# Kernel tuning notes

Hardware: AMD Instinct MI355X
Metric: run time of the kernel (lower is better)

The kernel has to match this reference:

```python
import jax, jax.numpy as jnp
import numpy as np

ALPHA = 4.0   # spikingjelly surrogate.Sigmoid default
TAU = 2.0
VTH = 1.0
EPS = 1e-5

@jax.custom_vjp
def spike(x):
    return (x >= 0.0).astype(x.dtype)

def _spike_fwd(x):
    return spike(x), x

def _spike_bwd(x, g):
    s = jax.nn.sigmoid(ALPHA * x)
    return (g * ALPHA * s * (1.0 - s),)

spike.defvjp(_spike_fwd, _spike_bwd)

def lif(x):
    # x: [T, B, N, C]; multi-step LIF, v_reset=0 hard reset, detach_reset=True
    def step(v, xt):
        v = v + (xt - v) / TAU          # charge
        s = spike(v - VTH)              # fire (surrogate grad)
        v = v * (1.0 - jax.lax.stop_gradient(s))  # hard reset, detached
        return v, s
    _, out = jax.lax.scan(step, jnp.zeros_like(x[0]), x)
    return out

def bn(x, gamma, beta):
    # BatchNorm1d in training mode: per-channel (last dim) over all other dims
    mu = x.mean(axis=(0, 1, 2), keepdims=True)
    var = x.var(axis=(0, 1, 2), keepdims=True)  # biased var, as torch BN uses for normalization
    return (x - mu) * jax.lax.rsqrt(var + EPS) * gamma + beta

def setup_inputs() -> dict:
    key = jax.random.key(0)
    ks = jax.random.split(key, 3)
    T, B, N, C, H = 4, 32, 1024, 256, 256
    x = jax.random.normal(ks[0], (T, B, N, C), dtype=jnp.float32)
    W1 = jax.random.normal(ks[1], (C, H), dtype=jnp.float32) * (1.0 / np.sqrt(C))
    W2 = jax.random.normal(ks[2], (H, C), dtype=jnp.float32) * (1.0 / np.sqrt(H))
    return {
        "x": x,
        "W1": W1, "b1": jnp.zeros((H,), jnp.float32),
        "gamma1": jnp.ones((H,), jnp.float32), "beta1": jnp.zeros((H,), jnp.float32),
        "W2": W2, "b2": jnp.zeros((C,), jnp.float32),
        "gamma2": jnp.ones((C,), jnp.float32), "beta2": jnp.zeros((C,), jnp.float32),
    }

def reference(x, W1, b1, gamma1, beta1, W2, b2, gamma2, beta2):
    # fc1: Linear -> BN (per-channel over T*B*N) -> multi-step LIF
    h = jnp.einsum('tbnc,ch->tbnh', x, W1) + b1
    h = lif(bn(h, gamma1, beta1))
    # fc2
    o = jnp.einsum('tbnh,ho->tbno', h, W2) + b2
    return lif(bn(o, gamma2, beta2))
```

## Files before the change

kernel.cpp:

```cpp
#include <hip/hip_runtime.h>


typedef __attribute__((ext_vector_type(8))) short bf16x8;
typedef __attribute__((ext_vector_type(8))) _Float16 f16x8;
typedef __attribute__((ext_vector_type(4))) _Float16 f16x4;
typedef __attribute__((ext_vector_type(4))) float f32x4;

__device__ __forceinline__ unsigned short f32_to_bf16_rne(float f) {
    unsigned int u = __builtin_bit_cast(unsigned int, f);
    u += 0x7FFFu + ((u >> 16) & 1u);
    return (unsigned short)(u >> 16);
}
__device__ __forceinline__ float bf16_to_f32(unsigned short h) {
    unsigned int u = ((unsigned int)h) << 16;
    return __builtin_bit_cast(float, u);
}

__global__ __launch_bounds__(256) void split_w1(const float* __restrict__ W1,
                                                _Float16* __restrict__ BhiT,
                                                _Float16* __restrict__ BloT) {
    int i = blockIdx.x * 256 + threadIdx.x;
    int k = i >> 8, n = i & 255;
    float w = W1[i];
    _Float16 hi = (_Float16)w;
    _Float16 lo = (_Float16)((w - (float)hi) * 4096.0f);
    BhiT[(size_t)n * 256 + k] = hi;
    BloT[(size_t)n * 256 + k] = lo;
}

__global__ __launch_bounds__(256) void split_w2(const float* __restrict__ W2,
                                                unsigned short* __restrict__ Bt) {
    int i = blockIdx.x * 256 + threadIdx.x;
    int k = i >> 8, n = i & 255;
    float w = W2[i];
    unsigned short hi = f32_to_bf16_rne(w);
    float r = w - bf16_to_f32(hi);
    unsigned short mid = f32_to_bf16_rne(r);
    float r2 = r - bf16_to_f32(mid);
    unsigned short lo = f32_to_bf16_rne(r2);
    Bt[(size_t)(0 * 256 + n) * 256 + k] = hi;
    Bt[(size_t)(1 * 256 + n) * 256 + k] = mid;
    Bt[(size_t)(2 * 256 + n) * 256 + k] = lo;
}

__global__ __launch_bounds__(512) void gemm1_mfma(const float* __restrict__ A,
                                                  const _Float16* __restrict__ Bhi,
                                                  const _Float16* __restrict__ Blo,
                                                  const float* __restrict__ bias,
                                                  float* __restrict__ C,
                                                  double* __restrict__ partial) {
    __shared__ __align__(16) _Float16 Ahi[128 * 256];
    __shared__ __align__(16) _Float16 Alo[128 * 256];
    const size_t m0 = (size_t)blockIdx.x * 128;
    const int tid = threadIdx.x;
    const int lane = tid & 63;
    const int wave = tid >> 6;
    const int wr = wave >> 2;
    const int wc = wave & 3;
    const int lrow = lane & 15, lchunk = lane >> 4;

    const _Float16* BhiB = Bhi + ((size_t)(64 * wc + lrow)) * 256 + lchunk * 8;
    const _Float16* BloB = Blo + ((size_t)(64 * wc + lrow)) * 256 + lchunk * 8;

    f16x8 bh[2][4], bl[2][4];
#define LOADB1(buf, kk)                                                   \
    _Pragma("unroll") for (int nf = 0; nf < 4; ++nf) {                    \
        bh[buf][nf] = *(const f16x8*)(BhiB + nf * 4096 + (kk) * 32);      \
        bl[buf][nf] = *(const f16x8*)(BloB + nf * 4096 + (kk) * 32);      \
    }

    LOADB1(0, 0)

    {
        const float* src = A + m0 * 256;
#pragma unroll
        for (int it = 0; it < 16; ++it) {
            unsigned i4 = (unsigned)(it * 512 + tid);
            float4 v = *(const float4*)(src + (size_t)i4 * 4);
            float f[4] = {v.x, v.y, v.z, v.w};
            f16x4 hi4, lo4;
#pragma unroll
            for (int e = 0; e < 4; ++e) {
                _Float16 hh = (_Float16)f[e];
                hi4[e] = hh;
                lo4[e] = (_Float16)((f[e] - (float)hh) * 4096.0f);
            }
            unsigned off = i4 * 8u;
            unsigned swz = off ^ (((off >> 9) & 7u) << 4);
            *(f16x4*)((char*)Ahi + swz) = hi4;
            *(f16x4*)((char*)Alo + swz) = lo4;
        }
    }
    __syncthreads();

    f32x4 acc0[4][4] = {}, acc1[4][4] = {};

#pragma unroll
    for (int k0 = 0; k0 < 8; ++k0) {
        const int cur = k0 & 1;
        if (k0 < 7) { LOADB1(cur ^ 1, k0 + 1) }
        f16x8 ah[4], al[4];
#pragma unroll
        for (int mf = 0; mf < 4; ++mf) {
            unsigned r = (unsigned)(64 * wr + 16 * mf + lrow);
            unsigned off = (r * 512u + (unsigned)(k0 * 64 + lchunk * 16)) ^ ((r & 7u) << 4);
            ah[mf] = *(const f16x8*)((const char*)Ahi + off);
            al[mf] = *(const f16x8*)((const char*)Alo + off);
        }
#pragma unroll
        for (int nf = 0; nf < 4; ++nf)
#pragma unroll
            for (int mf = 0; mf < 4; ++mf)
                acc0[mf][nf] = __builtin_amdgcn_mfma_f32_16x16x32_f16(
                    ah[mf], bh[cur][nf], acc0[mf][nf], 0, 0, 0);
#pragma unroll
        for (int nf = 0; nf < 4; ++nf)
#pragma unroll
            for (int mf = 0; mf < 4; ++mf)
                acc1[mf][nf] = __builtin_amdgcn_mfma_f32_16x16x32_f16(
                    ah[mf], bl[cur][nf], acc1[mf][nf], 0, 0, 0);
#pragma unroll
        for (int nf = 0; nf < 4; ++nf)
#pragma unroll
            for (int mf = 0; mf < 4; ++mf)
                acc1[mf][nf] = __builtin_amdgcn_mfma_f32_16x16x32_f16(
                    al[mf], bh[cur][nf], acc1[mf][nf], 0, 0, 0);
    }
#undef LOADB1

    const float UNSCALE = 1.0f / 4096.0f;
    double s[4], q[4];
#pragma unroll
    for (int nf = 0; nf < 4; ++nf) {
        int col = 64 * wc + 16 * nf + lrow;
        float bvv = bias[col];
        double ss = 0.0, qq = 0.0;
#pragma unroll
        for (int mf = 0; mf < 4; ++mf) {
            size_t rowb = m0 + 64 * wr + 16 * mf + 4 * lchunk;
#pragma unroll
            for (int e = 0; e < 4; ++e) {
                float hv = acc0[mf][nf][e] + acc1[mf][nf][e] * UNSCALE + bvv;
                C[(rowb + e) * 256 + col] = hv;
                ss += (double)hv;
                qq += (double)hv * (double)hv;
            }
        }
        s[nf] = ss;
        q[nf] = qq;
    }
#pragma unroll
    for (int nf = 0; nf < 4; ++nf) {
        s[nf] += __shfl_xor(s[nf], 16);
        s[nf] += __shfl_xor(s[nf], 32);
        q[nf] += __shfl_xor(q[nf], 16);
        q[nf] += __shfl_xor(q[nf], 32);
    }
    __syncthreads();
    double* shred = (double*)Ahi;
    if (lane < 16) {
#pragma unroll
        for (int nf = 0; nf < 4; ++nf) {
            shred[(wave * 4 + nf) * 16 + lane] = s[nf];
            shred[512 + (wave * 4 + nf) * 16 + lane] = q[nf];
        }
    }
    __syncthreads();
    if (wave < 4) {
        int nf = lane >> 4, lr = lane & 15;
        int col = 64 * wave + 16 * nf + lr;
        double ssum = shred[(wave * 4 + nf) * 16 + lr] +
                      shred[((4 + wave) * 4 + nf) * 16 + lr];
        double qsum = shred[512 + (wave * 4 + nf) * 16 + lr] +
                      shred[512 + ((4 + wave) * 4 + nf) * 16 + lr];
        partial[(size_t)col * 1024 + blockIdx.x] = ssum;
        partial[(size_t)(256 + col) * 1024 + blockIdx.x] = qsum;
    }
}

__global__ __launch_bounds__(512) void gemm2_mfma(const unsigned short* __restrict__ A,
                                                  const unsigned short* __restrict__ Bt,
                                                  const float* __restrict__ bias,
                                                  float* __restrict__ C,
                                                  double* __restrict__ partial) {
    __shared__ __align__(16) unsigned short Asw[128 * 256];
    const size_t m0 = (size_t)blockIdx.x * 128;
    const int tid = threadIdx.x;
    const int lane = tid & 63;
    const int wave = tid >> 6;
    const int wr = wave >> 2;
    const int wc = wave & 3;
    const int lrow = lane & 15, lchunk = lane >> 4;

    {
        const char* src = (const char*)(A + m0 * 256);
        char* dst = (char*)Asw;
#pragma unroll
        for (int it = 0; it < 8; ++it) {
            unsigned off = (unsigned)(it * 512 + tid) * 16u;
            float4 v = *(const float4*)(src + off);
            unsigned swz = off ^ (((off >> 9) & 7u) << 4);
            *(float4*)(dst + swz) = v;
        }
    }

    const unsigned short* Bbase =
        Bt + ((size_t)(64 * wc + lrow)) * 256 + lchunk * 8;

    bf16x8 bb[2][12];
#define LOADB(buf, kk)                                                        \
    _Pragma("unroll") for (int t = 0; t < 3; ++t)                             \
    _Pragma("unroll") for (int nf = 0; nf < 4; ++nf)                          \
        bb[buf][t * 4 + nf] = *(const bf16x8*)(Bbase + (size_t)t * 65536 +    \
                                               nf * 4096 + (kk) * 32);

    LOADB(0, 0)
    __syncthreads();

    f32x4 acc[4][4] = {};

#pragma unroll
    for (int k0 = 0; k0 < 8; ++k0) {
        const int cur = k0 & 1;
        if (k0 < 7) { LOADB(cur ^ 1, k0 + 1) }
        bf16x8 af[4];
#pragma unroll
        for (int mf = 0; mf < 4; ++mf) {
            unsigned r = (unsigned)(64 * wr + 16 * mf + lrow);
            unsigned off = r * 512u + (unsigned)(k0 * 64 + lchunk * 16);
            off ^= ((r & 7u) << 4);
            af[mf] = *(const bf16x8*)((const char*)Asw + off);
        }
#pragma unroll
        for (int t = 0; t < 3; ++t)
#pragma unroll
            for (int nf = 0; nf < 4; ++nf)
#pragma unroll
                for (int mf = 0; mf < 4; ++mf)
                    acc[mf][nf] = __builtin_amdgcn_mfma_f32_16x16x32_bf16(
                        af[mf], bb[cur][t * 4 + nf], acc[mf][nf], 0, 0, 0);
    }
#undef LOADB

    double s[4], q[4];
#pragma unroll
    for (int nf = 0; nf < 4; ++nf) {
        int col = 64 * wc + 16 * nf + lrow;
        float bvv = bias[col];
        double ss = 0.0, qq = 0.0;
#pragma unroll
        for (int mf = 0; mf < 4; ++mf) {
            size_t rowb = m0 + 64 * wr + 16 * mf + 4 * lchunk;
#pragma unroll
            for (int e = 0; e < 4; ++e) {
                float hv = acc[mf][nf][e] + bvv;
                C[(rowb + e) * 256 + col] = hv;
                ss += (double)hv;
                qq += (double)hv * (double)hv;
            }
        }
        s[nf] = ss;
        q[nf] = qq;
    }
#pragma unroll
    for (int nf = 0; nf < 4; ++nf) {
        s[nf] += __shfl_xor(s[nf], 16);
        s[nf] += __shfl_xor(s[nf], 32);
        q[nf] += __shfl_xor(q[nf], 16);
        q[nf] += __shfl_xor(q[nf], 32);
    }
    __syncthreads();
    double* shred = (double*)Asw;
    if (lane < 16) {
#pragma unroll
        for (int nf = 0; nf < 4; ++nf) {
            shred[(wave * 4 + nf) * 16 + lane] = s[nf];
            shred[512 + (wave * 4 + nf) * 16 + lane] = q[nf];
        }
    }
    __syncthreads();
    if (wave < 4) {
        int nf = lane >> 4, lr = lane & 15;
        int col = 64 * wave + 16 * nf + lr;
        double ssum = shred[(wave * 4 + nf) * 16 + lr] +
                      shred[((4 + wave) * 4 + nf) * 16 + lr];
        double qsum = shred[512 + (wave * 4 + nf) * 16 + lr] +
                      shred[512 + ((4 + wave) * 4 + nf) * 16 + lr];
        partial[(size_t)col * 1024 + blockIdx.x] = ssum;
        partial[(size_t)(256 + col) * 1024 + blockIdx.x] = qsum;
    }
}

__global__ __launch_bounds__(256) void finalize_stats(const double* __restrict__ partial,
                                                      const float* __restrict__ gamma,
                                                      const float* __restrict__ beta,
                                                      float2* __restrict__ ss,
                                                      int nblocks, double invM) {
    const int c = blockIdx.x;
    const int t = threadIdx.x;
    __shared__ double sh[256];
    __shared__ double sh2[256];
    double s = 0.0, s2 = 0.0;
    for (int b = t; b < nblocks; b += 256) {
        s += partial[(size_t)c * nblocks + b];
        s2 += partial[(size_t)(256 + c) * nblocks + b];
    }
    sh[t] = s;
    sh2[t] = s2;
    __syncthreads();
#pragma unroll
    for (int off = 128; off > 0; off >>= 1) {
        if (t < off) {
            sh[t] += sh[t + off];
            sh2[t] += sh2[t + off];
        }
        __syncthreads();
    }
    if (t == 0) {
        double mu = sh[0] * invM;
        double var = sh2[0] * invM - mu * mu;
        double rstd = 1.0 / sqrt(var + 1e-5);
        double sc = (double)gamma[c] * rstd;
        ss[c] = make_float2((float)sc, (float)((double)beta[c] - mu * sc));
    }
}

__global__ __launch_bounds__(256) void bnlif_bf16(const float* __restrict__ h,
                                                  const float2* __restrict__ ss,
                                                  unsigned short* __restrict__ out,
                                                  int slab4) {
    int t4 = blockIdx.x * 256 + threadIdx.x;
    if (t4 >= slab4) return;
    size_t idx = (size_t)t4 * 4;
    int c0 = (int)(idx & 255);
    float2 p0 = ss[c0], p1 = ss[c0 + 1], p2 = ss[c0 + 2], p3 = ss[c0 + 3];
    size_t slab = (size_t)slab4 * 4;
    float4 v = make_float4(0.f, 0.f, 0.f, 0.f);
#pragma unroll
    for (int t = 0; t < 4; ++t) {
        float4 hv = *(const float4*)(h + (size_t)t * slab + idx);
        float x0 = hv.x * p0.x + p0.y;
        float x1 = hv.y * p1.x + p1.y;
        float x2 = hv.z * p2.x + p2.y;
        float x3 = hv.w * p3.x + p3.y;
        v.x = v.x + (x0 - v.x) * 0.5f;
        v.y = v.y + (x1 - v.y) * 0.5f;
        v.z = v.z + (x2 - v.z) * 0.5f;
        v.w = v.w + (x3 - v.w) * 0.5f;
        ushort4 sp;
        sp.x = (v.x >= 1.0f) ? 0x3F80 : 0;
        sp.y = (v.y >= 1.0f) ? 0x3F80 : 0;
        sp.z = (v.z >= 1.0f) ? 0x3F80 : 0;
        sp.w = (v.w >= 1.0f) ? 0x3F80 : 0;
        v.x = (v.x >= 1.0f) ? 0.0f : v.x;
        v.y = (v.y >= 1.0f) ? 0.0f : v.y;
        v.z = (v.z >= 1.0f) ? 0.0f : v.z;
        v.w = (v.w >= 1.0f) ? 0.0f : v.w;
        *(ushort4*)(out + (size_t)t * slab + idx) = sp;
    }
}

__global__ __launch_bounds__(256) void bnlif_f32(const float* __restrict__ h,
                                                 const float2* __restrict__ ss,
                                                 float* __restrict__ out,
                                                 int slab4) {
    int t4 = blockIdx.x * 256 + threadIdx.x;
    if (t4 >= slab4) return;
    size_t idx = (size_t)t4 * 4;
    int c0 = (int)(idx & 255);
    float2 p0 = ss[c0], p1 = ss[c0 + 1], p2 = ss[c0 + 2], p3 = ss[c0 + 3];
    size_t slab = (size_t)slab4 * 4;
    float4 v = make_float4(0.f, 0.f, 0.f, 0.f);
#pragma unroll
    for (int t = 0; t < 4; ++t) {
        float4 hv = *(const float4*)(h + (size_t)t * slab + idx);
        float x0 = hv.x * p0.x + p0.y;
        float x1 = hv.y * p1.x + p1.y;
        float x2 = hv.z * p2.x + p2.y;
        float x3 = hv.w * p3.x + p3.y;
        v.x = v.x + (x0 - v.x) * 0.5f;
        v.y = v.y + (x1 - v.y) * 0.5f;
        v.z = v.z + (x2 - v.z) * 0.5f;
        v.w = v.w + (x3 - v.w) * 0.5f;
        float4 sp;
        sp.x = (v.x >= 1.0f) ? 1.0f : 0.0f;
        sp.y = (v.y >= 1.0f) ? 1.0f : 0.0f;
        sp.z = (v.z >= 1.0f) ? 1.0f : 0.0f;
        sp.w = (v.w >= 1.0f) ? 1.0f : 0.0f;
        v.x = (v.x >= 1.0f) ? 0.0f : v.x;
        v.y = (v.y >= 1.0f) ? 0.0f : v.y;
        v.z = (v.z >= 1.0f) ? 0.0f : v.z;
        v.w = (v.w >= 1.0f) ? 0.0f : v.w;
        *(float4*)(out + (size_t)t * slab + idx) = sp;
    }
}

extern "C" void kernel_launch(void* const* d_in, const int* in_sizes, int n_in,
                              void* d_out, int out_size, void* d_ws, size_t ws_size,
                              hipStream_t stream) {
    const float* x  = (const float*)d_in[0];
    const float* W1 = (const float*)d_in[1];
    const float* b1 = (const float*)d_in[2];
    const float* g1 = (const float*)d_in[3];
    const float* be1 = (const float*)d_in[4];
    const float* W2 = (const float*)d_in[5];
    const float* b2 = (const float*)d_in[6];
    const float* g2 = (const float*)d_in[7];
    const float* be2 = (const float*)d_in[8];
    float* out = (float*)d_out;

    const int M = in_sizes[0] / 256;
    const size_t hBytes = (size_t)M * 256 * 4;

    char* ws = (char*)d_ws;
    float* h = (float*)ws;
    unsigned short* s1b = (unsigned short*)(ws + hBytes);
    double* partial = (double*)(ws + hBytes + hBytes / 2);
    const int NB = 1024;
    unsigned short* W2catT = (unsigned short*)(ws + hBytes + hBytes / 2 + (size_t)NB * 512 * 8);
    float2* ss1 = (float2*)((char*)W2catT + 3 * 256 * 256 * 2);
    float2* ss2 = ss1 + 256;
    _Float16* W1hiT = (_Float16*)(ss2 + 256);
    _Float16* W1loT = W1hiT + 256 * 256;

    const int slab4 = M * 16;
    const double invM = 1.0 / (double)M;

    dim3 blk(256);

    split_w1<<<dim3(256), blk, 0, stream>>>(W1, W1hiT, W1loT);
    split_w2<<<dim3(256), blk, 0, stream>>>(W2, W2catT);

    gemm1_mfma<<<dim3(M / 128), dim3(512), 0, stream>>>(x, W1hiT, W1loT, b1, h, partial);
    finalize_stats<<<dim3(256), blk, 0, stream>>>(partial, g1, be1, ss1, NB, invM);
    bnlif_bf16<<<dim3(slab4 / 256), blk, 0, stream>>>(h, ss1, s1b, slab4);

    gemm2_mfma<<<dim3(M / 128), dim3(512), 0, stream>>>(s1b, W2catT, b2, h, partial);
    finalize_stats<<<dim3(256), blk, 0, stream>>>(partial, g2, be2, ss2, NB, invM);
    bnlif_f32<<<dim3(slab4 / 256), blk, 0, stream>>>(h, ss2, out, slab4);
}
```

Before: 338.4 us.

## Split gemm1 over N halves and stream A in double-buffered K chunks

gemm1 now launches twice as many blocks, each computing 128 rows by 128 output columns instead of all 256. A is staged through double-buffered 64-wide K chunks in LDS (64KB total instead of 128KB), with global loads issued one chunk ahead. B fragments are loaded directly per k-step instead of being register double-buffered. The aim is higher occupancy and overlap of the fp32 A loads and hi/lo splitting with MFMA work. The cost is that each A tile is read and split twice, and there are extra barriers per chunk.

```diff
diff --git a/kernel.cpp b/kernel.cpp
--- a/kernel.cpp
+++ b/kernel.cpp
@@ -43,101 +43,111 @@
     Bt[(size_t)(2 * 256 + n) * 256 + k] = lo;
 }
 
-__global__ __launch_bounds__(512) void gemm1_mfma(const float* __restrict__ A,
-                                                  const _Float16* __restrict__ Bhi,
-                                                  const _Float16* __restrict__ Blo,
-                                                  const float* __restrict__ bias,
-                                                  float* __restrict__ C,
-                                                  double* __restrict__ partial) {
-    __shared__ __align__(16) _Float16 Ahi[128 * 256];
-    __shared__ __align__(16) _Float16 Alo[128 * 256];
-    const size_t m0 = (size_t)blockIdx.x * 128;
+__global__ __launch_bounds__(512, 4) void gemm1_mfma(const float* __restrict__ A,
+                                                     const _Float16* __restrict__ Bhi,
+                                                     const _Float16* __restrict__ Blo,
+                                                     const float* __restrict__ bias,
+                                                     float* __restrict__ C,
+                                                     double* __restrict__ partial) {
+    __shared__ __align__(16) char Alds[65536];
+    const int bi = blockIdx.x >> 1;
+    const int bj = blockIdx.x & 1;
+    const size_t m0 = (size_t)bi * 128;
+    const int n0 = bj * 128;
     const int tid = threadIdx.x;
     const int lane = tid & 63;
     const int wave = tid >> 6;
-    const int wr = wave >> 2;
-    const int wc = wave & 3;
+    const int wr = wave >> 1;
+    const int wc = wave & 1;
     const int lrow = lane & 15, lchunk = lane >> 4;
 
-    const _Float16* BhiB = Bhi + ((size_t)(64 * wc + lrow)) * 256 + lchunk * 8;
-    const _Float16* BloB = Blo + ((size_t)(64 * wc + lrow)) * 256 + lchunk * 8;
-
-    f16x8 bh[2][4], bl[2][4];
-#define LOADB1(buf, kk)                                                   \
-    _Pragma("unroll") for (int nf = 0; nf < 4; ++nf) {                    \
-        bh[buf][nf] = *(const f16x8*)(BhiB + nf * 4096 + (kk) * 32);      \
-        bl[buf][nf] = *(const f16x8*)(BloB + nf * 4096 + (kk) * 32);      \
-    }
-
-    LOADB1(0, 0)
-
-    {
-        const float* src = A + m0 * 256;
-#pragma unroll
-        for (int it = 0; it < 16; ++it) {
-            unsigned i4 = (unsigned)(it * 512 + tid);
-            float4 v = *(const float4*)(src + (size_t)i4 * 4);
-            float f[4] = {v.x, v.y, v.z, v.w};
-            f16x4 hi4, lo4;
-#pragma unroll
-            for (int e = 0; e < 4; ++e) {
-                _Float16 hh = (_Float16)f[e];
-                hi4[e] = hh;
-                lo4[e] = (_Float16)((f[e] - (float)hh) * 4096.0f);
+    const int srow = tid >> 4, scolq = tid & 15;
+
+    float4 ld[4];
+#define LOADA(c)                                                              \
+    _Pragma("unroll") for (int it = 0; it < 4; ++it) {                        \
+        int row = it * 32 + srow;                                             \
+        ld[it] = *(const float4*)(A + (m0 + row) * 256 + (c) * 64 + scolq * 4); \
+    }
+#define WRITEA(buf)                                                           \
+    _Pragma("unroll") for (int it = 0; it < 4; ++it) {                        \
+        int row = it * 32 + srow;                                             \
+        float f0 = ld[it].x, f1 = ld[it].y, f2 = ld[it].z, f3 = ld[it].w;     \
+        f16x4 hi4, lo4;                                                       \
+        _Float16 h0 = (_Float16)f0; hi4[0] = h0; lo4[0] = (_Float16)((f0 - (float)h0) * 4096.0f); \
+        _Float16 h1 = (_Float16)f1; hi4[1] = h1; lo4[1] = (_Float16)((f1 - (float)h1) * 4096.0f); \
+        _Float16 h2 = (_Float16)f2; hi4[2] = h2; lo4[2] = (_Float16)((f2 - (float)h2) * 4096.0f); \
+        _Float16 h3 = (_Float16)f3; hi4[3] = h3; lo4[3] = (_Float16)((f3 - (float)h3) * 4096.0f); \
+        unsigned off = ((unsigned)row * 128u + (unsigned)scolq * 8u) ^ (((unsigned)row & 7u) << 4); \
+        *(f16x4*)(Alds + (buf) * 32768 + off) = hi4;                          \
+        *(f16x4*)(Alds + (buf) * 32768 + 16384 + off) = lo4;                  \
+    }
+
+    const _Float16* BhiB = Bhi + ((size_t)(n0 + 64 * wc + lrow)) * 256 + lchunk * 8;
+    const _Float16* BloB = Blo + ((size_t)(n0 + 64 * wc + lrow)) * 256 + lchunk * 8;
+
+    f32x4 acc0[2][4] = {}, acc1[2][4] = {};
+
+    LOADA(0)
+    WRITEA(0)
+    __syncthreads();
+    LOADA(1)
+
+#pragma unroll
+    for (int c = 0; c < 4; ++c) {
+        const int buf = c & 1;
+#pragma unroll
+        for (int ks = 0; ks < 2; ++ks) {
+            const int K0 = c * 64 + ks * 32;
+            f16x8 ah[2], al[2];
+#pragma unroll
+            for (int mf = 0; mf < 2; ++mf) {
+                unsigned r = (unsigned)(32 * wr + 16 * mf + lrow);
+                unsigned off = (r * 128u + (unsigned)(ks * 64 + lchunk * 16)) ^ ((r & 7u) << 4);
+                ah[mf] = *(const f16x8*)(Alds + buf * 32768 + off);
+                al[mf] = *(const f16x8*)(Alds + buf * 32768 + 16384 + off);
             }
-            unsigned off = i4 * 8u;
-            unsigned swz = off ^ (((off >> 9) & 7u) << 4);
-            *(f16x4*)((char*)Ahi + swz) = hi4;
-            *(f16x4*)((char*)Alo + swz) = lo4;
-        }
-    }
-    __syncthreads();
-
-    f32x4 acc0[4][4] = {}, acc1[4][4] = {};
-
-#pragma unroll
-    for (int k0 = 0; k0 < 8; ++k0) {
-        const int cur = k0 & 1;
-        if (k0 < 7) { LOADB1(cur ^ 1, k0 + 1) }
-        f16x8 ah[4], al[4];
-#pragma unroll
-        for (int mf = 0; mf < 4; ++mf) {
-            unsigned r = (unsigned)(64 * wr + 16 * mf + lrow);
-            unsigned off = (r * 512u + (unsigned)(k0 * 64 + lchunk * 16)) ^ ((r & 7u) << 4);
-            ah[mf] = *(const f16x8*)((const char*)Ahi + off);
-            al[mf] = *(const f16x8*)((const char*)Alo + off);
-        }
-#pragma unroll
-        for (int nf = 0; nf < 4; ++nf)
-#pragma unroll
-            for (int mf = 0; mf < 4; ++mf)
-                acc0[mf][nf] = __builtin_amdgcn_mfma_f32_16x16x32_f16(
-                    ah[mf], bh[cur][nf], acc0[mf][nf], 0, 0, 0);
-#pragma unroll
-        for (int nf = 0; nf < 4; ++nf)
-#pragma unroll
-            for (int mf = 0; mf < 4; ++mf)
-                acc1[mf][nf] = __builtin_amdgcn_mfma_f32_16x16x32_f16(
-                    ah[mf], bl[cur][nf], acc1[mf][nf], 0, 0, 0);
-#pragma unroll
-        for (int nf = 0; nf < 4; ++nf)
-#pragma unroll
-            for (int mf = 0; mf < 4; ++mf)
-                acc1[mf][nf] = __builtin_amdgcn_mfma_f32_16x16x32_f16(
-                    al[mf], bh[cur][nf], acc1[mf][nf], 0, 0, 0);
-    }
-#undef LOADB1
+            f16x8 bh[4], bl[4];
+#pragma unroll
+            for (int nf = 0; nf < 4; ++nf) bh[nf] = *(const f16x8*)(BhiB + nf * 4096 + K0);
+#pragma unroll
+            for (int nf = 0; nf < 4; ++nf) bl[nf] = *(const f16x8*)(BloB + nf * 4096 + K0);
+#pragma unroll
+            for (int nf = 0; nf < 4; ++nf)
+#pragma unroll
+                for (int mf = 0; mf < 2; ++mf)
+                    acc0[mf][nf] = __builtin_amdgcn_mfma_f32_16x16x32_f16(ah[mf], bh[nf], acc0[mf][nf], 0, 0, 0);
+#pragma unroll
+            for (int nf = 0; nf < 4; ++nf)
+#pragma unroll
+                for (int mf = 0; mf < 2; ++mf)
+                    acc1[mf][nf] = __builtin_amdgcn_mfma_f32_16x16x32_f16(ah[mf], bl[nf], acc1[mf][nf], 0, 0, 0);
+#pragma unroll
+            for (int nf = 0; nf < 4; ++nf)
+#pragma unroll
+                for (int mf = 0; mf < 2; ++mf)
+                    acc1[mf][nf] = __builtin_amdgcn_mfma_f32_16x16x32_f16(al[mf], bh[nf], acc1[mf][nf], 0, 0, 0);
+        }
+        if (c < 3) {
+            __syncthreads();
+            WRITEA((c + 1) & 1)
+            if (c < 2) { LOADA(c + 2) }
+            __syncthreads();
+        }
+    }
+#undef LOADA
+#undef WRITEA
 
     const float UNSCALE = 1.0f / 4096.0f;
     double s[4], q[4];
 #pragma unroll
     for (int nf = 0; nf < 4; ++nf) {
-        int col = 64 * wc + 16 * nf + lrow;
+        int col = n0 + 64 * wc + 16 * nf + lrow;
         float bvv = bias[col];
         double ss = 0.0, qq = 0.0;
 #pragma unroll
-        for (int mf = 0; mf < 4; ++mf) {
-            size_t rowb = m0 + 64 * wr + 16 * mf + 4 * lchunk;
+        for (int mf = 0; mf < 2; ++mf) {
+            size_t rowb = m0 + 32 * wr + 16 * mf + 4 * lchunk;
 #pragma unroll
             for (int e = 0; e < 4; ++e) {
                 float hv = acc0[mf][nf][e] + acc1[mf][nf][e] * UNSCALE + bvv;
@@ -157,7 +167,7 @@
         q[nf] += __shfl_xor(q[nf], 32);
     }
     __syncthreads();
-    double* shred = (double*)Ahi;
+    double* shred = (double*)Alds;
     if (lane < 16) {
 #pragma unroll
         for (int nf = 0; nf < 4; ++nf) {
@@ -166,15 +176,18 @@
         }
     }
     __syncthreads();
-    if (wave < 4) {
+    if (wave < 2) {
         int nf = lane >> 4, lr = lane & 15;
-        int col = 64 * wave + 16 * nf + lr;
-        double ssum = shred[(wave * 4 + nf) * 16 + lr] +
-                      shred[((4 + wave) * 4 + nf) * 16 + lr];
-        double qsum = shred[512 + (wave * 4 + nf) * 16 + lr] +
-                      shred[512 + ((4 + wave) * 4 + nf) * 16 + lr];
-        partial[(size_t)col * 1024 + blockIdx.x] = ssum;
-        partial[(size_t)(256 + col) * 1024 + blockIdx.x] = qsum;
+        int col_local = 64 * wave + 16 * nf + lr;
+        double ssum = 0.0, qsum = 0.0;
+#pragma unroll
+        for (int w = 0; w < 4; ++w) {
+            ssum += shred[((2 * w + wave) * 4 + nf) * 16 + lr];
+            qsum += shred[512 + ((2 * w + wave) * 4 + nf) * 16 + lr];
+        }
+        int c = n0 + col_local;
+        partial[(size_t)c * 1024 + bi] = ssum;
+        partial[(size_t)(256 + c) * 1024 + bi] = qsum;
     }
 }
 
@@ -431,7 +444,7 @@
     split_w1<<<dim3(256), blk, 0, stream>>>(W1, W1hiT, W1loT);
     split_w2<<<dim3(256), blk, 0, stream>>>(W2, W2catT);
 
-    gemm1_mfma<<<dim3(M / 128), dim3(512), 0, stream>>>(x, W1hiT, W1loT, b1, h, partial);
+    gemm1_mfma<<<dim3((M / 128) * 2), dim3(512), 0, stream>>>(x, W1hiT, W1loT, b1, h, partial);
     finalize_stats<<<dim3(256), blk, 0, stream>>>(partial, g1, be1, ss1, NB, invM);
     bnlif_bf16<<<dim3(slab4 / 256), blk, 0, stream>>>(h, ss1, s1b, slab4);
 
```

Result: slower. 528.5 us (+56.2%).

## Fuse first BN+LIF into gemm2 prologue and transpose partial-stats layout

Applied to the files above, without the earlier changes.

Removes the standalone bnlif_bf16 kernel and the bf16 spike buffer. gemm2 now loads the fp32 fc1 output for 32 (B,N) rows across all four timesteps, applies BN scale/shift and the LIF recurrence in registers, and writes the bf16 spikes straight into swizzled shared memory before the MFMA loop. Output rows are remapped so each block writes the same rows it read, which makes the in-place overwrite of h safe. The per-block stats partials switch to a block-major layout with coalesced writes and a matching finalize. The LIF update is also rewritten as (v+x)*0.5, which can change rounding slightly compared with the reference form.

```diff
diff --git a/kernel.cpp b/kernel.cpp
--- a/kernel.cpp
+++ b/kernel.cpp
@@ -173,18 +173,20 @@
                       shred[((4 + wave) * 4 + nf) * 16 + lr];
         double qsum = shred[512 + (wave * 4 + nf) * 16 + lr] +
                       shred[512 + ((4 + wave) * 4 + nf) * 16 + lr];
-        partial[(size_t)col * 1024 + blockIdx.x] = ssum;
-        partial[(size_t)(256 + col) * 1024 + blockIdx.x] = qsum;
-    }
-}
-
-__global__ __launch_bounds__(512) void gemm2_mfma(const unsigned short* __restrict__ A,
-                                                  const unsigned short* __restrict__ Bt,
-                                                  const float* __restrict__ bias,
-                                                  float* __restrict__ C,
-                                                  double* __restrict__ partial) {
+        partial[(size_t)blockIdx.x * 512 + col] = ssum;
+        partial[(size_t)blockIdx.x * 512 + 256 + col] = qsum;
+    }
+}
+
+__global__ __launch_bounds__(512) void gemm2_fused(const float* __restrict__ h,
+                                                   const float2* __restrict__ ss1,
+                                                   const unsigned short* __restrict__ Bt,
+                                                   const float* __restrict__ bias,
+                                                   float* __restrict__ C,
+                                                   double* __restrict__ partial,
+                                                   int bnRows) {
     __shared__ __align__(16) unsigned short Asw[128 * 256];
-    const size_t m0 = (size_t)blockIdx.x * 128;
+    const int bn0 = blockIdx.x * 32;
     const int tid = threadIdx.x;
     const int lane = tid & 63;
     const int wave = tid >> 6;
@@ -192,18 +194,6 @@
     const int wc = wave & 3;
     const int lrow = lane & 15, lchunk = lane >> 4;
 
-    {
-        const char* src = (const char*)(A + m0 * 256);
-        char* dst = (char*)Asw;
-#pragma unroll
-        for (int it = 0; it < 8; ++it) {
-            unsigned off = (unsigned)(it * 512 + tid) * 16u;
-            float4 v = *(const float4*)(src + off);
-            unsigned swz = off ^ (((off >> 9) & 7u) << 4);
-            *(float4*)(dst + swz) = v;
-        }
-    }
-
     const unsigned short* Bbase =
         Bt + ((size_t)(64 * wc + lrow)) * 256 + lchunk * 8;
 
@@ -215,6 +205,42 @@
                                                nf * 4096 + (kk) * 32);
 
     LOADB(0, 0)
+
+    {
+#pragma unroll
+        for (int it = 0; it < 4; ++it) {
+            int slot = it * 512 + tid;
+            int bn = slot >> 6;
+            int colq = slot & 63;
+            int c0 = colq * 4;
+            float2 p0 = ss1[c0], p1 = ss1[c0 + 1], p2 = ss1[c0 + 2], p3 = ss1[c0 + 3];
+            float4 v = make_float4(0.f, 0.f, 0.f, 0.f);
+#pragma unroll
+            for (int t = 0; t < 4; ++t) {
+                float4 hv = *(const float4*)(h + ((size_t)t * bnRows + bn0 + bn) * 256 + c0);
+                float x0 = hv.x * p0.x + p0.y;
+                float x1 = hv.y * p1.x + p1.y;
+                float x2 = hv.z * p2.x + p2.y;
+                float x3 = hv.w * p3.x + p3.y;
+                v.x = (v.x + x0) * 0.5f;
+                v.y = (v.y + x1) * 0.5f;
+                v.z = (v.z + x2) * 0.5f;
+                v.w = (v.w + x3) * 0.5f;
+                ushort4 sp;
+                sp.x = (v.x >= 1.0f) ? 0x3F80 : 0;
+                sp.y = (v.y >= 1.0f) ? 0x3F80 : 0;
+                sp.z = (v.z >= 1.0f) ? 0x3F80 : 0;
+                sp.w = (v.w >= 1.0f) ? 0x3F80 : 0;
+                v.x = (v.x >= 1.0f) ? 0.0f : v.x;
+                v.y = (v.y >= 1.0f) ? 0.0f : v.y;
+                v.z = (v.z >= 1.0f) ? 0.0f : v.z;
+                v.w = (v.w >= 1.0f) ? 0.0f : v.w;
+                unsigned row = (unsigned)(t * 32 + bn);
+                unsigned off = (row * 512u + (unsigned)colq * 8u) ^ ((row & 7u) << 4);
+                *(ushort4*)((char*)Asw + off) = sp;
+            }
+        }
+    }
     __syncthreads();
 
     f32x4 acc[4][4] = {};
@@ -250,11 +276,13 @@
         double ss = 0.0, qq = 0.0;
 #pragma unroll
         for (int mf = 0; mf < 4; ++mf) {
-            size_t rowb = m0 + 64 * wr + 16 * mf + 4 * lchunk;
+            int Lbase = 64 * wr + 16 * mf + 4 * lchunk;
 #pragma unroll
             for (int e = 0; e < 4; ++e) {
+                int L = Lbase + e;
+                size_t G = (size_t)(L >> 5) * bnRows + bn0 + (L & 31);
                 float hv = acc[mf][nf][e] + bvv;
-                C[(rowb + e) * 256 + col] = hv;
+                C[G * 256 + col] = hv;
                 ss += (double)hv;
                 qq += (double)hv * (double)hv;
             }
@@ -286,8 +314,8 @@
                       shred[((4 + wave) * 4 + nf) * 16 + lr];
         double qsum = shred[512 + (wave * 4 + nf) * 16 + lr] +
                       shred[512 + ((4 + wave) * 4 + nf) * 16 + lr];
-        partial[(size_t)col * 1024 + blockIdx.x] = ssum;
-        partial[(size_t)(256 + col) * 1024 + blockIdx.x] = qsum;
+        partial[(size_t)blockIdx.x * 512 + col] = ssum;
+        partial[(size_t)blockIdx.x * 512 + 256 + col] = qsum;
     }
 }
 
@@ -302,8 +330,8 @@
     __shared__ double sh2[256];
     double s = 0.0, s2 = 0.0;
     for (int b = t; b < nblocks; b += 256) {
-        s += partial[(size_t)c * nblocks + b];
-        s2 += partial[(size_t)(256 + c) * nblocks + b];
+        s += partial[(size_t)b * 512 + c];
+        s2 += partial[(size_t)b * 512 + 256 + c];
     }
     sh[t] = s;
     sh2[t] = s2;
@@ -322,41 +350,6 @@
         double rstd = 1.0 / sqrt(var + 1e-5);
         double sc = (double)gamma[c] * rstd;
         ss[c] = make_float2((float)sc, (float)((double)beta[c] - mu * sc));
-    }
-}
-
-__global__ __launch_bounds__(256) void bnlif_bf16(const float* __restrict__ h,
-                                                  const float2* __restrict__ ss,
-                                                  unsigned short* __restrict__ out,
-                                                  int slab4) {
-    int t4 = blockIdx.x * 256 + threadIdx.x;
-    if (t4 >= slab4) return;
-    size_t idx = (size_t)t4 * 4;
-    int c0 = (int)(idx & 255);
-    float2 p0 = ss[c0], p1 = ss[c0 + 1], p2 = ss[c0 + 2], p3 = ss[c0 + 3];
-    size_t slab = (size_t)slab4 * 4;
-    float4 v = make_float4(0.f, 0.f, 0.f, 0.f);
-#pragma unroll
-    for (int t = 0; t < 4; ++t) {
-        float4 hv = *(const float4*)(h + (size_t)t * slab + idx);
-        float x0 = hv.x * p0.x + p0.y;
-        float x1 = hv.y * p1.x + p1.y;
-        float x2 = hv.z * p2.x + p2.y;
-        float x3 = hv.w * p3.x + p3.y;
-        v.x = v.x + (x0 - v.x) * 0.5f;
-        v.y = v.y + (x1 - v.y) * 0.5f;
-        v.z = v.z + (x2 - v.z) * 0.5f;
-        v.w = v.w + (x3 - v.w) * 0.5f;
-        ushort4 sp;
-        sp.x = (v.x >= 1.0f) ? 0x3F80 : 0;
-        sp.y = (v.y >= 1.0f) ? 0x3F80 : 0;
-        sp.z = (v.z >= 1.0f) ? 0x3F80 : 0;
-        sp.w = (v.w >= 1.0f) ? 0x3F80 : 0;
-        v.x = (v.x >= 1.0f) ? 0.0f : v.x;
-        v.y = (v.y >= 1.0f) ? 0.0f : v.y;
-        v.z = (v.z >= 1.0f) ? 0.0f : v.z;
-        v.w = (v.w >= 1.0f) ? 0.0f : v.w;
-        *(ushort4*)(out + (size_t)t * slab + idx) = sp;
     }
 }
 
@@ -378,10 +371,10 @@
         float x1 = hv.y * p1.x + p1.y;
         float x2 = hv.z * p2.x + p2.y;
         float x3 = hv.w * p3.x + p3.y;
-        v.x = v.x + (x0 - v.x) * 0.5f;
-        v.y = v.y + (x1 - v.y) * 0.5f;
-        v.z = v.z + (x2 - v.z) * 0.5f;
-        v.w = v.w + (x3 - v.w) * 0.5f;
+        v.x = (v.x + x0) * 0.5f;
+        v.y = (v.y + x1) * 0.5f;
+        v.z = (v.z + x2) * 0.5f;
+        v.w = (v.w + x3) * 0.5f;
         float4 sp;
         sp.x = (v.x >= 1.0f) ? 1.0f : 0.0f;
         sp.y = (v.y >= 1.0f) ? 1.0f : 0.0f;
@@ -410,14 +403,13 @@
     float* out = (float*)d_out;
 
     const int M = in_sizes[0] / 256;
+    const int bnRows = M / 4;
     const size_t hBytes = (size_t)M * 256 * 4;
 
     char* ws = (char*)d_ws;
     float* h = (float*)ws;
-    unsigned short* s1b = (unsigned short*)(ws + hBytes);
-    double* partial = (double*)(ws + hBytes + hBytes / 2);
-    const int NB = 1024;
-    unsigned short* W2catT = (unsigned short*)(ws + hBytes + hBytes / 2 + (size_t)NB * 512 * 8);
+    double* partial = (double*)(ws + hBytes);
+    unsigned short* W2catT = (unsigned short*)(ws + hBytes + (size_t)1024 * 512 * 8);
     float2* ss1 = (float2*)((char*)W2catT + 3 * 256 * 256 * 2);
     float2* ss2 = ss1 + 256;
     _Float16* W1hiT = (_Float16*)(ss2 + 256);
@@ -432,10 +424,9 @@
     split_w2<<<dim3(256), blk, 0, stream>>>(W2, W2catT);
 
     gemm1_mfma<<<dim3(M / 128), dim3(512), 0, stream>>>(x, W1hiT, W1loT, b1, h, partial);
-    finalize_stats<<<dim3(256), blk, 0, stream>>>(partial, g1, be1, ss1, NB, invM);
-    bnlif_bf16<<<dim3(slab4 / 256), blk, 0, stream>>>(h, ss1, s1b, slab4);
-
-    gemm2_mfma<<<dim3(M / 128), dim3(512), 0, stream>>>(s1b, W2catT, b2, h, partial);
-    finalize_stats<<<dim3(256), blk, 0, stream>>>(partial, g2, be2, ss2, NB, invM);
+    finalize_stats<<<dim3(256), blk, 0, stream>>>(partial, g1, be1, ss1, M / 128, invM);
+
+    gemm2_fused<<<dim3(bnRows / 32), dim3(512), 0, stream>>>(h, ss1, W2catT, b2, h, partial, bnRows);
+    finalize_stats<<<dim3(256), blk, 0, stream>>>(partial, g2, be2, ss2, bnRows / 32, invM);
     bnlif_f32<<<dim3(slab4 / 256), blk, 0, stream>>>(h, ss2, out, slab4);
 }
```

Result: faster. 329.4 us (-2.7%).
